# Performance work log

Measured on AMD Instinct MI355X. Metric: run time of the kernel, lower is better.

## Reference

```python
import jax, jax.numpy as jnp
import numpy as np
from math import comb

N_INPUT, N_HIDDEN, N_LATENT = 2, 1024, 16
T, B = 320, 192
DEG = N_LATENT // 2 - 1          # 7
NPTS = DEG + 1                   # 8 control points
LAT = N_LATENT + N_LATENT // 2   # 24

_COMB = jnp.array([comb(DEG, i) for i in range(NPTS)], dtype=jnp.float32)
_I = jnp.arange(NPTS, dtype=jnp.float32)


def setup_inputs() -> dict:
    key = jax.random.key(0)
    ks = jax.random.split(key, 24)
    H = N_HIDDEN
    w = lambda k, shape, sc: (jax.random.normal(k, shape, jnp.float32) * sc)
    return dict(
        x=jax.random.normal(ks[0], (T, B, N_INPUT), jnp.float32),
        latent_ctrlpt=jax.random.normal(ks[1], (B, N_LATENT), jnp.float32),
        latent_ratw=jax.random.uniform(ks[2], (B, N_LATENT // 2), jnp.float32, 0.1, 1.0),
        # h0/c0 projection linears (forward/backward directions)
        W_hf=w(ks[3], (H, LAT), 0.2), b_hf=jnp.zeros((H,), jnp.float32),
        W_hb=w(ks[4], (H, LAT), 0.2), b_hb=jnp.zeros((H,), jnp.float32),
        W_cf=w(ks[5], (H, LAT), 0.2), b_cf=jnp.zeros((H,), jnp.float32),
        W_cb=w(ks[6], (H, LAT), 0.2), b_cb=jnp.zeros((H,), jnp.float32),
        # bi-LSTM weights, PyTorch gate order (i, f, g, o)
        W_ih_f=w(ks[7], (4 * H, N_INPUT), 0.03), W_hh_f=w(ks[8], (4 * H, H), 0.03),
        b_ih_f=jnp.zeros((4 * H,), jnp.float32), b_hh_f=jnp.zeros((4 * H,), jnp.float32),
        W_ih_b=w(ks[9], (4 * H, N_INPUT), 0.03), W_hh_b=w(ks[10], (4 * H, H), 0.03),
        b_ih_b=jnp.zeros((4 * H,), jnp.float32), b_hh_b=jnp.zeros((4 * H,), jnp.float32),
        # t-logits head
        W_log=w(ks[11], (1, 2 * H), 0.03), b_log=jnp.zeros((1,), jnp.float32),
    )


def _lstm_dir(x_tm, h0, c0, W_ih, W_hh, b_ih, b_hh, reverse):
    # x_tm: (T, B, in). Precompute input projection once (compute-efficient).
    xs = jnp.einsum('tbi,gi->tbg', x_tm, W_ih) + b_ih + b_hh  # (T, B, 4H)

    def step(carry, xt):
        h, c = carry
        g = xt + h @ W_hh.T
        i, f, gg, o = jnp.split(g, 4, axis=-1)
        c = jax.nn.sigmoid(f) * c + jax.nn.sigmoid(i) * jnp.tanh(gg)
        h = jax.nn.sigmoid(o) * jnp.tanh(c)
        return (h, c), h

    _, hs = jax.lax.scan(step, (h0, c0), xs, reverse=reverse)
    return hs  # (T, B, H)


def reference(x, latent_ctrlpt, latent_ratw,
              W_hf, b_hf, W_hb, b_hb, W_cf, b_cf, W_cb, b_cb,
              W_ih_f, W_hh_f, b_ih_f, b_hh_f,
              W_ih_b, W_hh_b, b_ih_b, b_hh_b,
              W_log, b_log):
    latent = jnp.concatenate([latent_ctrlpt, latent_ratw], axis=1)  # (B, LAT)
    h0f = jnp.tanh(latent @ W_hf.T + b_hf)
    h0b = jnp.tanh(latent @ W_hb.T + b_hb)
    c0f = jnp.tanh(latent @ W_cf.T + b_cf)
    c0b = jnp.tanh(latent @ W_cb.T + b_cb)

    hf = _lstm_dir(x, h0f, c0f, W_ih_f, W_hh_f, b_ih_f, b_hh_f, reverse=False)
    hb = _lstm_dir(x, h0b, c0b, W_ih_b, W_hh_b, b_ih_b, b_hh_b, reverse=True)
    out = jnp.concatenate([hf, hb], axis=-1)           # (T, B, 2H)
    out = jnp.transpose(out, (1, 0, 2))                # batch_first (B, T, 2H)

    logits = (out @ W_log.T + b_log)[..., 0]           # (B, T)
    ts = jnp.cumsum(jax.nn.softmax(logits, axis=1), axis=1)  # (B, T) in (0, 1]

    P = latent_ctrlpt.reshape(-1, NPTS, 2)             # (B, NPTS, 2)
    r = latent_ratw.reshape(-1, NPTS)                  # (B, NPTS)

    # Rational Bezier curve, batched over B and T (replaces per-sample loop)
    t = ts[..., None]                                   # (B, T, 1)
    basis = _COMB * t ** _I * (1.0 - t) ** (DEG - _I)   # (B, T, NPTS)
    num = basis * r[:, None, :]
    w = num / num.sum(-1, keepdims=True)
    curves = jnp.einsum('btn,bnd->btd', w, P)           # (B, T, 2)

    # mean of squared consecutive control-point distances, averaged over batch
    d2 = ((P[:, 1:, :] - P[:, :-1, :]) ** 2).sum(-1)    # (B, NPTS-1)
    reg = d2.mean()
    return curves, reg
```

## Files before the change

kernel.cpp:

```cpp
#include <hip/hip_runtime.h>
#include <stdint.h>

#define T_STEPS 320
#define BATCH   192
#define HID     1024
#define NBLK    256

typedef unsigned short u16;
typedef __bf16 bf16x8 __attribute__((ext_vector_type(8)));
typedef float  f32x4  __attribute__((ext_vector_type(4)));
typedef unsigned int u32x4 __attribute__((ext_vector_type(4)));

#define OFF_BAR      0u
#define OFF_PART     16384u
#define MEMSET_BYTES 3948544u
#define OFF_C0       3948544u
#define OFF_H        5521408u
#define OFF_WPACK    7094272u
#define OFF_COEF     23871488u
#define WS_NEED      24002560u

#define DMP_OFF_B    131072
#define DMP_WK_STRIDE 1632
#define DYN_LDS      157200

__device__ __forceinline__ u16 f2bf(float f) {
  unsigned u = __float_as_uint(f);
  unsigned r = (u + 0x7FFFu + ((u >> 16) & 1u)) >> 16;
  return (u16)r;
}
__device__ __forceinline__ float sigm(float x)   { return 1.f / (1.f + __expf(-x)); }
__device__ __forceinline__ float tanh_f(float x) { return 1.f - 2.f / (1.f + __expf(2.f * x)); }

__global__ void pack_k(const float* __restrict__ Whhf, const float* __restrict__ Whhb,
                       u16* __restrict__ wpack)
{
  int lin = blockIdx.x * 256 + threadIdx.x;
  int lane = lin & 63;
  int cg   = (lin >> 6) & 3;
  int ks   = (lin >> 8) & 31;
  int jsl  = (lin >> 13) & 63;
  int dir  = (lin >> 19) & 1;
  int col  = cg * 16 + (lane & 15);
  int R    = (col & 3) * 1024 + jsl * 16 + (col >> 2);
  int kb   = ks * 32 + (lane >> 4) * 8;
  const float* W = dir ? Whhb : Whhf;
  const float* src = W + (size_t)R * 1024 + kb;
  unsigned w[4];
  #pragma unroll
  for (int e = 0; e < 4; ++e) {
    unsigned lo = f2bf(src[2 * e]);
    unsigned hi = f2bf(src[2 * e + 1]);
    w[e] = lo | (hi << 16);
  }
  *((uint4*)(wpack + (size_t)lin * 8)) = make_uint4(w[0], w[1], w[2], w[3]);
}

__global__ void coef_k(const float* __restrict__ Wihf, const float* __restrict__ bihf,
                       const float* __restrict__ bhhf,
                       const float* __restrict__ Wihb, const float* __restrict__ bihb,
                       const float* __restrict__ bhhb, float* __restrict__ coef)
{
  int id  = blockIdx.x * 256 + threadIdx.x;
  int col = id & 63;
  int jsl = (id >> 6) & 63;
  int dir = (id >> 12) & 1;
  int R   = (col & 3) * 1024 + jsl * 16 + (col >> 2);
  const float* Wih = dir ? Wihb : Wihf;
  const float* bi  = dir ? bihb : bihf;
  const float* bh  = dir ? bhhb : bhhf;
  float4 v;
  v.x = Wih[(size_t)R * 2 + 0];
  v.y = Wih[(size_t)R * 2 + 1];
  v.z = bi[R] + bh[R];
  v.w = 0.f;
  ((float4*)coef)[id] = v;
}

__global__ void init_k(const float* __restrict__ ctrl, const float* __restrict__ ratw,
                       const float* __restrict__ Whf, const float* __restrict__ bhf,
                       const float* __restrict__ Whb, const float* __restrict__ bhb,
                       const float* __restrict__ Wcf, const float* __restrict__ bcf,
                       const float* __restrict__ Wcb, const float* __restrict__ bcb,
                       u16* hb, float* c0)
{
  int idx = blockIdx.x * 256 + threadIdx.x;
  int m = blockIdx.y;
  int b = idx >> 10;
  int h = idx & 1023;
  const float* W  = (m == 0) ? Whf : (m == 1) ? Whb : (m == 2) ? Wcf : Wcb;
  const float* bi = (m == 0) ? bhf : (m == 1) ? bhb : (m == 2) ? bcf : bcb;
  float acc = bi[h];
  const float* wr = W + h * 24;
  #pragma unroll
  for (int k = 0; k < 16; ++k) acc += wr[k] * ctrl[b * 16 + k];
  #pragma unroll
  for (int k = 0; k < 8; ++k)  acc += wr[16 + k] * ratw[b * 8 + k];
  acc = tanh_f(acc);
  if (m < 2) hb[((size_t)(m * 2 + 0) * BATCH + b) * HID + h] = f2bf(acc);
  else       c0[((size_t)(m - 2) * BATCH + b) * HID + h] = acc;
}


#define ALD(S, OB) \
  asm volatile("global_load_dwordx4 %0, %1, off offset:" #OB " sc0 sc1" : "=v"(aq[S][0]) : "v"(ab0)); \
  asm volatile("global_load_dwordx4 %0, %1, off offset:" #OB " sc0 sc1" : "=v"(aq[S][1]) : "v"(ab1)); \
  asm volatile("global_load_dwordx4 %0, %1, off offset:" #OB " sc0 sc1" : "=v"(aq[S][2]) : "v"(ab2));

#define BLDS(P, C) { \
  bv[P][0] = *(const bf16x8*)(bWl + (C) * 2048 + 0);   \
  bv[P][1] = *(const bf16x8*)(bWl + (C) * 2048 + 512); \
  bv[P][2] = *(const bf16x8*)(bWl + (C) * 2048 + 1024);\
  bv[P][3] = *(const bf16x8*)(bWl + (C) * 2048 + 1536); }

#define WB(n) \
  asm volatile("s_waitcnt vmcnt(" #n ")" ::: "memory"); \
  __builtin_amdgcn_sched_barrier(0);

#define MM(C, P) { \
  _Pragma("unroll") \
  for (int mt_ = 0; mt_ < 3; ++mt_) { \
    bf16x8 a_ = __builtin_bit_cast(bf16x8, aq[C][mt_]); \
    _Pragma("unroll") \
    for (int n_ = 0; n_ < 4; ++n_) { \
      acc[mt_][n_] = __builtin_amdgcn_mfma_f32_16x16x32_bf16(a_, bv[P][n_], acc[mt_][n_], 0, 0, 0); \
    } \
  } }

#define HST(PT, VL) asm volatile("global_store_short %0, %1, off sc0 sc1" :: "v"(PT), "v"(VL) : "memory")

__launch_bounds__(512, 1)
__global__ void lstm_persist(const float* __restrict__ x,
                             const float* __restrict__ wlog,
                             float* part,
                             const float* __restrict__ c0,
                             u16* hb,
                             const u16* __restrict__ wpack,
                             const float* __restrict__ coef,
                             unsigned* bar)
{
  extern __shared__ char lds[];
  u16*   Wlds = (u16*)lds;
  float* DMP  = (float*)(lds + DMP_OFF_B);
  int*   ldsflag = (int*)(lds + DMP_OFF_B + 26112);

  const int tid   = threadIdx.x;
  const int bid   = blockIdx.x;
  const int dir   = bid >> 7;
  const int bhalf = (bid >> 6) & 1;
  const int jsl   = bid & 63;
  const int wave  = tid >> 6;
  const int lane  = tid & 63;
  const int wm    = wave >> 2;
  const int wk    = wave & 3;
  const int grp   = dir * 2 + bhalf;
  const int q4    = (lane >> 4) * 4;
  const int cl    = lane & 15;

  if (tid == 0) *ldsflag = 0;

  {
    const uint4* wsrc = (const uint4*)wpack + (size_t)(dir * 64 + jsl) * 8192;
    uint4* wdst = (uint4*)Wlds;
    #pragma unroll
    for (int i = 0; i < 16; ++i) wdst[tid + i * 512] = wsrc[tid + i * 512];
  }

  const int j    = tid & 15;
  const int rloc = tid >> 4;
  const bool pw  = (tid < 384);
  const int jglob = jsl * 16 + j;
  float4 cf0, cf1, cf2, cf3;
  {
    const float4* cp = (const float4*)coef + ((dir * 64 + jsl) * 64 + j * 4);
    cf0 = cp[0]; cf1 = cp[1]; cf2 = cp[2]; cf3 = cp[3];
  }
  const float wlg = wlog[dir * 1024 + jglob];

  float creg[4];
  int   bgm[4];
  #pragma unroll
  for (int p = 0; p < 4; ++p) {
    int bg = bhalf * 96 + p * 24 + rloc;
    bgm[p]  = bg;
    creg[p] = pw ? c0[((size_t)dir * BATCH + bg) * HID + jglob] : 0.f;
  }

  const int arow0 = bhalf * 96 + wm * 48 + 0 * 16 + cl;
  const int arow1 = arow0 + 16;
  const int arow2 = arow0 + 32;
  const int koff  = wk * 256 + (lane >> 4) * 8;
  const u16* bWl  = Wlds + (size_t)wk * 16384 + lane * 8;

  float* pbase = part + ((size_t)(dir * 8 + (jsl & 7)) * BATCH) * T_STEPS;

  unsigned* gflags = bar + grp * 1024;
  unsigned* myflag = gflags + jsl * 16;
  const unsigned* pollp = gflags + lane * 16;

  float lpv[4];
  int   lpo[4];

  __syncthreads();

  for (int s = 0; s < T_STEPS; ++s) {
    const int rbuf = s & 1;
    const u16* hsrc = hb + ((size_t)(dir * 2 + rbuf)) * BATCH * HID;
    u16*       hdst = hb + ((size_t)(dir * 2 + (rbuf ^ 1))) * BATCH * HID;
    const u16* ab0 = hsrc + (size_t)arow0 * HID + koff;
    const u16* ab1 = hsrc + (size_t)arow1 * HID + koff;
    const u16* ab2 = hsrc + (size_t)arow2 * HID + koff;

    f32x4 acc[3][4];
    #pragma unroll
    for (int mt = 0; mt < 3; ++mt)
      #pragma unroll
      for (int n = 0; n < 4; ++n)
        acc[mt][n] = (f32x4){0.f, 0.f, 0.f, 0.f};

    u32x4  aq[8][3];
    bf16x8 bv[2][4];

    ALD(0, 0)   ALD(1, 64)  ALD(2, 128) ALD(3, 192)
    ALD(4, 256) ALD(5, 320) ALD(6, 384) ALD(7, 448)

    BLDS(0, 0)
    BLDS(1, 1) WB(21) MM(0, 0)
    BLDS(0, 2) WB(18) MM(1, 1)
    BLDS(1, 3) WB(15) MM(2, 0)
    BLDS(0, 4) WB(12) MM(3, 1)
    BLDS(1, 5) WB(9)  MM(4, 0)
    BLDS(0, 6) WB(6)  MM(5, 1)
    BLDS(1, 7) WB(3)  MM(6, 0)
               WB(0)  MM(7, 1)

    const int t_x = dir ? (T_STEPS - 1 - s) : s;

    #pragma unroll
    for (int p = 0; p < 4; ++p) {
      if (wm == (p >> 1)) {
        const int plo = (p & 1) * 24;
        float* dst = DMP + wk * DMP_WK_STRIDE;
        #pragma unroll
        for (int mt = 0; mt < 3; ++mt)
          #pragma unroll
          for (int n = 0; n < 4; ++n)
            #pragma unroll
            for (int r = 0; r < 4; ++r) {
              int row = mt * 16 + q4 + r;
              if (row >= plo && row < plo + 24)
                dst[(row - plo) * 68 + n * 16 + cl] = acc[mt][n][r];
            }
      }
      __syncthreads();

      if (pw) {
        const int ga = rloc * 68 + (j >> 2) * 16 + (j & 3) * 4;
        f32x4 p0 = *(const f32x4*)(DMP + 0 * DMP_WK_STRIDE + ga);
        f32x4 p1 = *(const f32x4*)(DMP + 1 * DMP_WK_STRIDE + ga);
        f32x4 p2 = *(const f32x4*)(DMP + 2 * DMP_WK_STRIDE + ga);
        f32x4 p3 = *(const f32x4*)(DMP + 3 * DMP_WK_STRIDE + ga);
        f32x4 g4 = (p0 + p1) + (p2 + p3);
        int bg = bgm[p];
        float2 xv = *(const float2*)(x + ((size_t)t_x * BATCH + bg) * 2);
        float pi = g4[0] + cf0.x * xv.x + cf0.y * xv.y + cf0.z;
        float pf = g4[1] + cf1.x * xv.x + cf1.y * xv.y + cf1.z;
        float pg = g4[2] + cf2.x * xv.x + cf2.y * xv.y + cf2.z;
        float po = g4[3] + cf3.x * xv.x + cf3.y * xv.y + cf3.z;
        float ig = sigm(pi), fg = sigm(pf), gv = tanh_f(pg), og = sigm(po);
        float c = fg * creg[p] + ig * gv;
        creg[p] = c;
        float h = og * tanh_f(c);
        u16* hp = hdst + (size_t)bg * HID + jglob;
        unsigned hv = (unsigned)f2bf(h);
        HST(hp, hv);
        float lp = h * wlg;
        lp += __shfl_xor(lp, 1);
        lp += __shfl_xor(lp, 2);
        lp += __shfl_xor(lp, 4);
        lp += __shfl_xor(lp, 8);
        lpv[p] = lp;
        lpo[p] = bg * T_STEPS + t_x;
      }
      __syncthreads();
    }

    asm volatile("s_waitcnt vmcnt(0)" ::: "memory");
    __syncthreads();

    if (pw && j == 0) {
      atomicAdd(&pbase[lpo[0]], lpv[0]);
      atomicAdd(&pbase[lpo[1]], lpv[1]);
      atomicAdd(&pbase[lpo[2]], lpv[2]);
      atomicAdd(&pbase[lpo[3]], lpv[3]);
    }

    if (tid == 0) {
      unsigned nv = (unsigned)(s + 1);
      asm volatile("global_store_dword %0, %1, off sc0 sc1" :: "v"(myflag), "v"(nv) : "memory");
    }
    if (wave == 0) {
      const unsigned tgt = (unsigned)(s + 1);
      long guard = 0;
      for (;;) {
        unsigned fv;
        asm volatile("global_load_dword %0, %1, off sc0 sc1" : "=v"(fv) : "v"(pollp));
        asm volatile("s_waitcnt vmcnt(0)" ::: "memory");
        if (__all(fv >= tgt)) break;
        if (++guard > (1L << 20)) { if (lane == 0) *ldsflag = 1; break; }
        __builtin_amdgcn_s_sleep(1);
      }
    }
    __syncthreads();
    if (*ldsflag) return;
  }
}

__global__ void post_k(const float* __restrict__ part, const float* __restrict__ ctrl,
                       const float* __restrict__ ratw, float* __restrict__ out)
{
  __shared__ float sh[T_STEPS + 64];
  const int b = blockIdx.x;
  const int t = threadIdx.x;
  float l = 0.f;
  #pragma unroll
  for (int p = 0; p < 16; ++p)
    l += part[((size_t)p * BATCH + b) * T_STEPS + t];
  sh[t] = l;
  __syncthreads();
  if (t < 64) {
    float mm = sh[t];
    for (int i = t + 64; i < T_STEPS; i += 64) mm = fmaxf(mm, sh[i]);
    #pragma unroll
    for (int o = 32; o; o >>= 1) mm = fmaxf(mm, __shfl_xor(mm, o));
    if (t == 0) sh[T_STEPS] = mm;
  }
  __syncthreads();
  const float m = sh[T_STEPS];
  float e = __expf(l - m);
  __syncthreads();
  sh[t] = e;
  __syncthreads();
  for (int off = 1; off < T_STEPS; off <<= 1) {
    float v = (t >= off) ? sh[t - off] : 0.f;
    __syncthreads();
    sh[t] += v;
    __syncthreads();
  }
  const float total = sh[T_STEPS - 1];
  const float ts = sh[t] / total;

  float px[8], py[8], rr[8];
  #pragma unroll
  for (int n = 0; n < 8; ++n) {
    px[n] = ctrl[b * 16 + 2 * n];
    py[n] = ctrl[b * 16 + 2 * n + 1];
    rr[n] = ratw[b * 8 + n];
  }
  const float C[8] = {1.f, 7.f, 21.f, 35.f, 35.f, 21.f, 7.f, 1.f};
  float tp[8], up[8];
  tp[0] = 1.f; up[0] = 1.f;
  const float u = 1.f - ts;
  #pragma unroll
  for (int n = 1; n < 8; ++n) { tp[n] = tp[n - 1] * ts; up[n] = up[n - 1] * u; }
  float den = 0.f, nx = 0.f, ny = 0.f;
  #pragma unroll
  for (int n = 0; n < 8; ++n) {
    float w = C[n] * tp[n] * up[7 - n] * rr[n];
    den += w; nx += w * px[n]; ny += w * py[n];
  }
  out[(b * T_STEPS + t) * 2 + 0] = nx / den;
  out[(b * T_STEPS + t) * 2 + 1] = ny / den;

  if (b == 0) {
    __syncthreads();
    if (t < BATCH) {
      float s2 = 0.f;
      #pragma unroll
      for (int n = 0; n < 7; ++n) {
        float dx = ctrl[t * 16 + 2 * n + 2] - ctrl[t * 16 + 2 * n + 0];
        float dy = ctrl[t * 16 + 2 * n + 3] - ctrl[t * 16 + 2 * n + 1];
        s2 += dx * dx + dy * dy;
      }
      sh[t] = s2;
    }
    __syncthreads();
    if (t == 0) {
      float tot = 0.f;
      for (int i = 0; i < BATCH; ++i) tot += sh[i];
      out[BATCH * T_STEPS * 2] = tot / (float)(BATCH * 7);
    }
  }
}

extern "C" void kernel_launch(void* const* d_in, const int* in_sizes, int n_in,
                              void* d_out, int out_size, void* d_ws, size_t ws_size,
                              hipStream_t stream)
{
  const float* x    = (const float*)d_in[0];
  const float* ctrl = (const float*)d_in[1];
  const float* ratw = (const float*)d_in[2];
  const float* Whf  = (const float*)d_in[3];
  const float* bhf  = (const float*)d_in[4];
  const float* Whb  = (const float*)d_in[5];
  const float* bhb  = (const float*)d_in[6];
  const float* Wcf  = (const float*)d_in[7];
  const float* bcf  = (const float*)d_in[8];
  const float* Wcb  = (const float*)d_in[9];
  const float* bcb  = (const float*)d_in[10];
  const float* Wihf = (const float*)d_in[11];
  const float* Whhf = (const float*)d_in[12];
  const float* bihf = (const float*)d_in[13];
  const float* bhhf = (const float*)d_in[14];
  const float* Wihb = (const float*)d_in[15];
  const float* Whhb = (const float*)d_in[16];
  const float* bihb = (const float*)d_in[17];
  const float* bhhb = (const float*)d_in[18];
  const float* Wlog = (const float*)d_in[19];
  float* out = (float*)d_out;
  char*  ws  = (char*)d_ws;
  if (ws_size < (size_t)WS_NEED) return;

  unsigned* bar    = (unsigned*)(ws + OFF_BAR);
  float*    part   = (float*)(ws + OFF_PART);
  float*    c0     = (float*)(ws + OFF_C0);
  u16*      hb     = (u16*)(ws + OFF_H);
  u16*      wpack  = (u16*)(ws + OFF_WPACK);
  float*    coef   = (float*)(ws + OFF_COEF);

  hipMemsetAsync(ws, 0, MEMSET_BYTES, stream);
  pack_k<<<4096, 256, 0, stream>>>(Whhf, Whhb, wpack);
  coef_k<<<32, 256, 0, stream>>>(Wihf, bihf, bhhf, Wihb, bihb, bhhb, coef);
  init_k<<<dim3(768, 4), 256, 0, stream>>>(ctrl, ratw, Whf, bhf, Whb, bhb,
                                           Wcf, bcf, Wcb, bcb, hb, c0);
  hipFuncSetAttribute((const void*)lstm_persist,
                      hipFuncAttributeMaxDynamicSharedMemorySize, DYN_LDS);
  lstm_persist<<<NBLK, 512, DYN_LDS, stream>>>(x, Wlog, part, c0, hb, wpack, coef, bar);
  post_k<<<BATCH, T_STEPS, 0, stream>>>(part, ctrl, ratw, out);
}
```

Before: 3.722 ms.

## Store full hidden-state history per step to allow cached h loads

When the workspace is large enough, each timestep writes h into a fresh panel (321 panels per direction) instead of ping-ponging two buffers. Because no address is ever rewritten, the per-step h loads can drop the sc0 sc1 cache-bypass bits and go through the normal cache hierarchy without risk of reading stale data from a reused buffer. This costs about 250 MB of extra workspace and more distinct addresses touched, and it falls back to the old double-buffer path when the workspace is too small.

```diff
diff --git a/kernel.cpp b/kernel.cpp
--- a/kernel.cpp
+++ b/kernel.cpp
@@ -19,6 +19,10 @@
 #define OFF_WPACK    7094272u
 #define OFF_COEF     23871488u
 #define WS_NEED      24002560u
+#define OFF_HT       24002560u
+#define PANEL_ELEMS  196608u
+#define DIR_ELEMS    (321u * PANEL_ELEMS)
+#define WS_NEED_BIG  (OFF_HT + 2ull * DIR_ELEMS * 2ull)
 
 #define DMP_OFF_B    131072
 #define DMP_WK_STRIDE 1632
@@ -82,7 +86,7 @@
                        const float* __restrict__ Whb, const float* __restrict__ bhb,
                        const float* __restrict__ Wcf, const float* __restrict__ bcf,
                        const float* __restrict__ Wcb, const float* __restrict__ bcb,
-                       u16* hb, float* c0)
+                       u16* hb, float* c0, size_t hstride)
 {
   int idx = blockIdx.x * 256 + threadIdx.x;
   int m = blockIdx.y;
@@ -97,15 +101,20 @@
   #pragma unroll
   for (int k = 0; k < 8; ++k)  acc += wr[16 + k] * ratw[b * 8 + k];
   acc = tanh_f(acc);
-  if (m < 2) hb[((size_t)(m * 2 + 0) * BATCH + b) * HID + h] = f2bf(acc);
+  if (m < 2) hb[(size_t)m * hstride + (size_t)b * HID + h] = f2bf(acc);
   else       c0[((size_t)(m - 2) * BATCH + b) * HID + h] = acc;
 }
 
 
-#define ALD(S, OB) \
+#define ALD_B(S, OB) \
   asm volatile("global_load_dwordx4 %0, %1, off offset:" #OB " sc0 sc1" : "=v"(aq[S][0]) : "v"(ab0)); \
   asm volatile("global_load_dwordx4 %0, %1, off offset:" #OB " sc0 sc1" : "=v"(aq[S][1]) : "v"(ab1)); \
   asm volatile("global_load_dwordx4 %0, %1, off offset:" #OB " sc0 sc1" : "=v"(aq[S][2]) : "v"(ab2));
+
+#define ALD_C(S, OB) \
+  asm volatile("global_load_dwordx4 %0, %1, off offset:" #OB : "=v"(aq[S][0]) : "v"(ab0)); \
+  asm volatile("global_load_dwordx4 %0, %1, off offset:" #OB : "=v"(aq[S][1]) : "v"(ab1)); \
+  asm volatile("global_load_dwordx4 %0, %1, off offset:" #OB : "=v"(aq[S][2]) : "v"(ab2));
 
 #define BLDS(P, C) { \
   bv[P][0] = *(const bf16x8*)(bWl + (C) * 2048 + 0);   \
@@ -129,6 +138,7 @@
 
 #define HST(PT, VL) asm volatile("global_store_short %0, %1, off sc0 sc1" :: "v"(PT), "v"(VL) : "memory")
 
+template<int HIST>
 __launch_bounds__(512, 1)
 __global__ void lstm_persist(const float* __restrict__ x,
                              const float* __restrict__ wlog,
@@ -204,9 +214,16 @@
   __syncthreads();
 
   for (int s = 0; s < T_STEPS; ++s) {
-    const int rbuf = s & 1;
-    const u16* hsrc = hb + ((size_t)(dir * 2 + rbuf)) * BATCH * HID;
-    u16*       hdst = hb + ((size_t)(dir * 2 + (rbuf ^ 1))) * BATCH * HID;
+    const u16* hsrc;
+    u16*       hdst;
+    if constexpr (HIST) {
+      hsrc = hb + (size_t)dir * DIR_ELEMS + (size_t)s * PANEL_ELEMS;
+      hdst = hb + (size_t)dir * DIR_ELEMS + (size_t)(s + 1) * PANEL_ELEMS;
+    } else {
+      const int rbuf = s & 1;
+      hsrc = hb + (size_t)(dir * 2 + rbuf) * BATCH * HID;
+      hdst = hb + (size_t)(dir * 2 + (rbuf ^ 1)) * BATCH * HID;
+    }
     const u16* ab0 = hsrc + (size_t)arow0 * HID + koff;
     const u16* ab1 = hsrc + (size_t)arow1 * HID + koff;
     const u16* ab2 = hsrc + (size_t)arow2 * HID + koff;
@@ -221,8 +238,13 @@
     u32x4  aq[8][3];
     bf16x8 bv[2][4];
 
-    ALD(0, 0)   ALD(1, 64)  ALD(2, 128) ALD(3, 192)
-    ALD(4, 256) ALD(5, 320) ALD(6, 384) ALD(7, 448)
+    if constexpr (HIST) {
+      ALD_C(0, 0)   ALD_C(1, 64)  ALD_C(2, 128) ALD_C(3, 192)
+      ALD_C(4, 256) ALD_C(5, 320) ALD_C(6, 384) ALD_C(7, 448)
+    } else {
+      ALD_B(0, 0)   ALD_B(1, 64)  ALD_B(2, 128) ALD_B(3, 192)
+      ALD_B(4, 256) ALD_B(5, 320) ALD_B(6, 384) ALD_B(7, 448)
+    }
 
     BLDS(0, 0)
     BLDS(1, 1) WB(21) MM(0, 0)
@@ -421,20 +443,32 @@
   char*  ws  = (char*)d_ws;
   if (ws_size < (size_t)WS_NEED) return;
 
+  const bool big = (ws_size >= (size_t)WS_NEED_BIG);
+
   unsigned* bar    = (unsigned*)(ws + OFF_BAR);
   float*    part   = (float*)(ws + OFF_PART);
   float*    c0     = (float*)(ws + OFF_C0);
-  u16*      hb     = (u16*)(ws + OFF_H);
+  u16*      hsmall = (u16*)(ws + OFF_H);
+  u16*      hbig   = (u16*)(ws + OFF_HT);
   u16*      wpack  = (u16*)(ws + OFF_WPACK);
   float*    coef   = (float*)(ws + OFF_COEF);
+
+  u16*   hb      = big ? hbig : hsmall;
+  size_t hstride = big ? (size_t)DIR_ELEMS : (size_t)2 * BATCH * HID;
 
   hipMemsetAsync(ws, 0, MEMSET_BYTES, stream);
   pack_k<<<4096, 256, 0, stream>>>(Whhf, Whhb, wpack);
   coef_k<<<32, 256, 0, stream>>>(Wihf, bihf, bhhf, Wihb, bihb, bhhb, coef);
   init_k<<<dim3(768, 4), 256, 0, stream>>>(ctrl, ratw, Whf, bhf, Whb, bhb,
-                                           Wcf, bcf, Wcb, bcb, hb, c0);
-  hipFuncSetAttribute((const void*)lstm_persist,
-                      hipFuncAttributeMaxDynamicSharedMemorySize, DYN_LDS);
-  lstm_persist<<<NBLK, 512, DYN_LDS, stream>>>(x, Wlog, part, c0, hb, wpack, coef, bar);
+                                           Wcf, bcf, Wcb, bcb, hb, c0, hstride);
+  if (big) {
+    hipFuncSetAttribute((const void*)lstm_persist<1>,
+                        hipFuncAttributeMaxDynamicSharedMemorySize, DYN_LDS);
+    lstm_persist<1><<<NBLK, 512, DYN_LDS, stream>>>(x, Wlog, part, c0, hb, wpack, coef, bar);
+  } else {
+    hipFuncSetAttribute((const void*)lstm_persist<0>,
+                        hipFuncAttributeMaxDynamicSharedMemorySize, DYN_LDS);
+    lstm_persist<0><<<NBLK, 512, DYN_LDS, stream>>>(x, Wlog, part, c0, hb, wpack, coef, bar);
+  }
   post_k<<<BATCH, T_STEPS, 0, stream>>>(part, ctrl, ratw, out);
 }
```

Result: no change. 3.717 ms (-0.1%).
